# Performance work log

Hardware: AMD Instinct MI355X
Metric: run time of the kernel (lower is better)

## Reference

```python
import jax, jax.numpy as jnp
import numpy as np

N_FFT = 2048
HOP = 512
WIN_LENGTH = 2048
B, C, T, F = 8, 1, 2048, N_FFT // 2 + 1
LENGTH = HOP * (T - 1)  # 1048064


def _window():
    # scipy/librosa hann with fftbins=True (periodic); win_length == n_fft so pad_center is a no-op
    n = np.arange(WIN_LENGTH)
    return 0.5 - 0.5 * np.cos(2.0 * np.pi * n / WIN_LENGTH)


def _idft_mats():
    k = np.arange(N_FFT)
    ang = 2.0 * np.pi * np.outer(k, k) / N_FFT
    w = _window()
    Mr = np.cos(ang) / N_FFT * w[:, None]
    Mi = np.sin(ang) / N_FFT * w[:, None]
    return jnp.asarray(Mr, jnp.float32), jnp.asarray(Mi, jnp.float32)


_MR, _MI = _idft_mats()


def _window_sumsquare(n_frames):
    # librosa.filters.window_sumsquare with norm=None
    win_sq = _window() ** 2
    total = N_FFT + HOP * (n_frames - 1)
    ws = np.zeros(total)
    idx = (np.arange(n_frames)[:, None] * HOP + np.arange(N_FFT)).ravel()
    np.add.at(ws, idx, np.tile(win_sq, n_frames))
    return jnp.asarray(np.clip(ws, 1e-8, np.inf), jnp.float32)


def setup_inputs() -> dict:
    key = jax.random.key(0)
    k1, k2 = jax.random.split(key)
    real_stft = jax.random.normal(k1, (B, C, T, F), dtype=jnp.float32)
    imag_stft = jax.random.normal(k2, (B, C, T, F), dtype=jnp.float32)
    return {"real_stft": real_stft, "imag_stft": imag_stft, "length": LENGTH}


def reference(real_stft, imag_stft, length):
    b, c, t, f = real_stft.shape
    r = jnp.swapaxes(real_stft, 2, 3)   # (B, C, F, T)
    im = jnp.swapaxes(imag_stft, 2, 3)
    # 'reverse' conv: pick bins n_fft//2-1 .. 1 (conjugate-symmetric half)
    rev = slice(N_FFT // 2 - 1, 0, -1)
    full_r = jnp.concatenate([r, r[:, :, rev, :]], axis=2)        # (B, C, n_fft, T)
    full_i = jnp.concatenate([im, -im[:, :, rev, :]], axis=2)
    # windowed IDFT (real part of inverse transform), as the 1x1-conv matmuls do
    s = (jnp.einsum('ab,xcbt->xcta', _MR, full_r)
         - jnp.einsum('ab,xcbt->xcta', _MI, full_i))              # (B, C, T, n_fft)
    total = N_FFT + HOP * (t - 1)
    idx = jnp.arange(t)[:, None] * HOP + jnp.arange(N_FFT)        # (T, n_fft)
    # overlap-add (replaces the identity-kernel ConvTranspose2d)
    y = jnp.zeros((b, c, total), dtype=s.dtype).at[:, :, idx].add(s)
    y = y / _window_sumsquare(t)                                   # window-sum normalization
    start = N_FFT // 2                                             # center=True
    avail = total - start
    y = jax.lax.dynamic_slice_in_dim(y, start, min(length, avail), axis=2)
    if y.shape[-1] < length:
        y = jnp.pad(y, ((0, 0), (0, 0), (0, length - y.shape[-1])))
    return y  # (B, C, length)
```

## Files before the change

### kernel.cpp

```cpp
#include <hip/hip_runtime.h>

#define NFFT    2048
#define HOPSZ   512
#define BATCH   8
#define TFRAMES 2048
#define FBINS   1025
#define OUTLEN  1048064
#define TOTALP  1050112
#define MROWS   16384

__device__ __forceinline__ float bf2f(unsigned short h) {
    return __uint_as_float(((unsigned)h) << 16);
}

__device__ __forceinline__ float2 cmul(float2 a, float2 b) {
    return float2{a.x * b.x - a.y * b.y, a.x * b.y + a.y * b.x};
}
__device__ __forceinline__ float2 cadd(float2 a, float2 b) { return float2{a.x + b.x, a.y + b.y}; }
__device__ __forceinline__ float2 csub(float2 a, float2 b) { return float2{a.x - b.x, a.y - b.y}; }
__device__ __forceinline__ float2 cjmul(float2 a) { return float2{-a.y, a.x}; }

#define IDFT4(y0, y1, y2, y3, x0, x1, x2, x3) do {                         \
    float2 t0 = cadd(x0, x2), t1 = csub(x0, x2);                           \
    float2 t2 = cadd(x1, x3), t3 = cjmul(csub(x1, x3));                    \
    y0 = cadd(t0, t2); y2 = csub(t0, t2);                                  \
    y1 = cadd(t1, t3); y3 = csub(t1, t3); } while (0)

__device__ __forceinline__ void idft16(float2* y, const float2* x) {
    const float c1 = 0.92387953251128674f, s1 = 0.38268343236508977f;
    const float r2 = 0.70710678118654752f;
    float2 A[16];
    #pragma unroll
    for (int jb = 0; jb < 4; ++jb)
        IDFT4(A[jb * 4 + 0], A[jb * 4 + 1], A[jb * 4 + 2], A[jb * 4 + 3],
              x[jb], x[4 + jb], x[8 + jb], x[12 + jb]);
    A[4 + 1]  = cmul(A[4 + 1],  float2{c1, s1});
    A[4 + 2]  = cmul(A[4 + 2],  float2{r2, r2});
    A[4 + 3]  = cmul(A[4 + 3],  float2{s1, c1});
    A[8 + 1]  = cmul(A[8 + 1],  float2{r2, r2});
    A[8 + 2]  = cjmul(A[8 + 2]);
    A[8 + 3]  = cmul(A[8 + 3],  float2{-r2, r2});
    A[12 + 1] = cmul(A[12 + 1], float2{s1, c1});
    A[12 + 2] = cmul(A[12 + 2], float2{-r2, r2});
    A[12 + 3] = cmul(A[12 + 3], float2{-c1, -s1});
    #pragma unroll
    for (int ra = 0; ra < 4; ++ra)
        IDFT4(y[ra], y[ra + 4], y[ra + 8], y[ra + 12],
              A[ra], A[4 + ra], A[8 + ra], A[12 + ra]);
}

__global__ void build_tabs(float2* __restrict__ wt) {
    int n = blockIdx.x * 256 + threadIdx.x;
    const float s = 1.0f / 2048.0f;
    if (n < 1024)
        wt[n] = float2{(0.5f - 0.5f * cospif((float)(2 * n)     * (1.0f / 1024.0f))) * s,
                       (0.5f - 0.5f * cospif((float)(2 * n + 1) * (1.0f / 1024.0f))) * s};
}

__global__ __launch_bounds__(128) void fft_frames(
    const float* __restrict__ re, const float* __restrict__ im,
    const float2* __restrict__ wt,
    unsigned short* __restrict__ Y)
{
    __shared__ float2 tb[2][1024];

    const int tid   = threadIdx.x;
    const int lane  = tid & 63;
    const int wv    = tid >> 6;
    const int frame = blockIdx.x * 2 + wv;
    const int b     = frame >> 11;
    const int t     = frame & (TFRAMES - 1);
    const float* rr = re + (size_t)frame * FBINS;
    const float* ii = im + (size_t)frame * FBINS;

    const float2 packb = float2{cospif((float)lane * (1.0f / 1024.0f)),
                                sinpif((float)lane * (1.0f / 1024.0f))};
    const float2 base2 = cmul(packb, packb);

    const float wkc[16] = { 1.0f, 0.98078528040323044f, 0.92387953251128674f, 0.83146961230254524f,
                            0.70710678118654752f, 0.55557023301960222f, 0.38268343236508977f, 0.19509032201612827f,
                            0.0f, -0.19509032201612827f, -0.38268343236508977f, -0.55557023301960222f,
                            -0.70710678118654752f, -0.83146961230254524f, -0.92387953251128674f, -0.98078528040323044f };
    const float wks[16] = { 0.0f, 0.19509032201612827f, 0.38268343236508977f, 0.55557023301960222f,
                            0.70710678118654752f, 0.83146961230254524f, 0.92387953251128674f, 0.98078528040323044f,
                            1.0f, 0.98078528040323044f, 0.92387953251128674f, 0.83146961230254524f,
                            0.70710678118654752f, 0.55557023301960222f, 0.38268343236508977f, 0.19509032201612827f };

    float2 zz[16];
    #pragma unroll
    for (int k1 = 0; k1 < 16; ++k1) {
        const int m = 64 * k1 + lane;
        float Xr = rr[m],        Xi = ii[m];
        float Cr = rr[1024 - m], Ni = ii[1024 - m];
        float2 W = cmul(packb, float2{wkc[k1], wks[k1]});
        float Er = Xr + Cr, Ei = Xi - Ni;
        float Or = Xr - Cr, Oi = Xi + Ni;
        float2 z = float2{Er - (W.x * Oi + W.y * Or), Ei + (W.x * Or - W.y * Oi)};
        if (k1 == 0 && lane == 0)
            z = float2{Xr + Cr, Xr - Cr};
        zz[k1] = z;
    }

    float2 A[16];
    idft16(A, zz);

    {
        float2 w = base2;
        A[1] = cmul(A[1], w);
        #pragma unroll
        for (int n1 = 2; n1 < 16; ++n1) { w = cmul(w, base2); A[n1] = cmul(A[n1], w); }
    }

    {
        float4* rowp = (float4*)&tb[wv][lane * 16];
        #pragma unroll
        for (int j = 0; j < 8; ++j) {
            float2 e = A[2 * j], o = A[2 * j + 1];
            rowp[(j + lane) & 7] = float4{e.x, e.y, o.x, o.y};
        }
    }
    asm volatile("s_waitcnt lgkmcnt(0)" ::: "memory");
    __builtin_amdgcn_sched_barrier(0);

    const int q   = lane >> 4;
    const int n1r = lane & 15;
    float2 D[16];
    #pragma unroll
    for (int c1 = 0; c1 < 16; ++c1) {
        const int row = 4 * c1 + q;
        D[c1] = tb[wv][row * 16 + (((n1r >> 1) + row) & 7) * 2 + (n1r & 1)];
    }

    float2 E[16];
    idft16(E, D);

    {
        float2 bq = (q == 0) ? float2{1.0f, 0.0f}
                  : (q == 1) ? float2{0.99518472667219693f, 0.09801714032956060f}
                  : (q == 2) ? float2{0.98078528040323044f, 0.19509032201612827f}
                             : float2{0.95694033573220886f, 0.29028467725446237f};
        float2 w = bq;
        E[1] = cmul(E[1], w);
        #pragma unroll
        for (int v1 = 2; v1 < 16; ++v1) { w = cmul(w, bq); E[v1] = cmul(E[v1], w); }
    }

    unsigned short* Yb = Y + ((size_t)(b * 4 + (t & 3))) * TOTALP + t * HOPSZ;
    const int v2 = ((q & 1) << 1) | (q >> 1);
    const int nbase = n1r + (v2 << 8);
    #pragma unroll
    for (int v1 = 0; v1 < 16; ++v1) {
        float2 mine = E[v1];
        float2 oth  = float2{__shfl_xor(mine.x, 32), __shfl_xor(mine.y, 32)};
        float2 G    = (lane < 32) ? cadd(mine, oth) : csub(oth, mine);
        float2 o2   = float2{__shfl_xor(G.x, 16), __shfl_xor(G.y, 16)};
        float2 res;
        if (q == 0)      res = cadd(G, o2);
        else if (q == 1) res = csub(o2, G);
        else if (q == 2) res = float2{G.x - o2.y, G.y + o2.x};
        else             res = float2{o2.x + G.y, o2.y - G.x};
        const int n = nbase + (v1 << 4);
        const float2 wp = wt[n];
        const float lo = res.x * wp.x, hi = res.y * wp.y;
        unsigned pack;
        asm("v_cvt_pk_bf16_f32 %0, %1, %2" : "=v"(pack) : "v"(lo), "v"(hi));
        *(unsigned*)(Yb + 2 * n) = pack;
    }
}

__global__ __launch_bounds__(256) void final_pass(
    const unsigned short* __restrict__ Y,
    const float2*         __restrict__ wt,
    float*                __restrict__ out)
{
    const int tx = blockIdx.x * 256 + threadIdx.x;
    if (tx >= OUTLEN / 8) return;
    const int b  = blockIdx.y;
    const int n0 = tx * 8;
    const int p0 = n0 + 1024;
    int tmin = (p0 - 1536) >> 9;  if (tmin < 0) tmin = 0;
    int tmax = p0 >> 9;           if (tmax > TFRAMES - 1) tmax = TFRAMES - 1;

    float acc[8], ws[8];
    #pragma unroll
    for (int j = 0; j < 8; ++j) { acc[j] = 0.0f; ws[j] = 0.0f; }

    for (int t = tmin; t <= tmax; ++t) {
        const int a0 = p0 - t * HOPSZ;
        const uint4 pv = *(const uint4*)(Y + ((size_t)(b * 4 + (t & 3))) * TOTALP + p0);
        const unsigned pw[4] = {pv.x, pv.y, pv.z, pv.w};
        #pragma unroll
        for (int j = 0; j < 4; ++j) {
            acc[2 * j]     += bf2f((unsigned short)(pw[j] & 0xffffu));
            acc[2 * j + 1] += bf2f((unsigned short)(pw[j] >> 16));
        }
        #pragma unroll
        for (int j = 0; j < 4; ++j) {
            float2 w = wt[(a0 >> 1) + j];
            ws[2 * j]     += w.x * w.x;
            ws[2 * j + 1] += w.y * w.y;
        }
    }
    const float S2 = (1.0f / 2048.0f) * (1.0f / 2048.0f);
    float r[8];
    #pragma unroll
    for (int j = 0; j < 8; ++j) r[j] = acc[j] * S2 / fmaxf(ws[j], 2.4e-15f);
    float4* o = (float4*)(out + (size_t)b * OUTLEN + n0);
    o[0] = float4{r[0], r[1], r[2], r[3]};
    o[1] = float4{r[4], r[5], r[6], r[7]};
}

extern "C" void kernel_launch(void* const* d_in, const int* in_sizes, int n_in,
                              void* d_out, int out_size, void* d_ws, size_t ws_size,
                              hipStream_t stream) {
    const float* re = (const float*)d_in[0];
    const float* im = (const float*)d_in[1];
    float* out = (float*)d_out;

    char* ws = (char*)d_ws;
    unsigned short* Y  = (unsigned short*)(ws);
    float2*         wt = (float2*)       (ws + 67207168);

    build_tabs<<<dim3(4),          256, 0, stream>>>(wt);
    fft_frames<<<dim3(MROWS / 2),  128, 0, stream>>>(re, im, wt, Y);
    final_pass<<<dim3(512, BATCH), 256, 0, stream>>>(Y, wt, out);
}
```

Measured before the change: 76.41 us.

## Process two frames per wavefront with interleaved FFT stages

Each wavefront now handles two STFT frames instead of one, and the grid is halved to match. The code is split into helper stages so the second frame's global loads and first-stage FFT run between the first frame's LDS transpose and its second stage, overlapping memory latency with compute. The explicit waitcnt/sched barrier is dropped and the twiddle constants move to __constant__ memory. In exchange, register pressure rises under the (128,4) launch bound, which risks spills and lower occupancy.

```diff
diff --git a/kernel.cpp b/kernel.cpp
--- a/kernel.cpp
+++ b/kernel.cpp
@@ -49,6 +49,15 @@
               A[ra], A[4 + ra], A[8 + ra], A[12 + ra]);
 }
 
+__constant__ float WKC[16] = { 1.0f, 0.98078528040323044f, 0.92387953251128674f, 0.83146961230254524f,
+                               0.70710678118654752f, 0.55557023301960222f, 0.38268343236508977f, 0.19509032201612827f,
+                               0.0f, -0.19509032201612827f, -0.38268343236508977f, -0.55557023301960222f,
+                               -0.70710678118654752f, -0.83146961230254524f, -0.92387953251128674f, -0.98078528040323044f };
+__constant__ float WKS[16] = { 0.0f, 0.19509032201612827f, 0.38268343236508977f, 0.55557023301960222f,
+                               0.70710678118654752f, 0.83146961230254524f, 0.92387953251128674f, 0.98078528040323044f,
+                               1.0f, 0.98078528040323044f, 0.92387953251128674f, 0.83146961230254524f,
+                               0.70710678118654752f, 0.55557023301960222f, 0.38268343236508977f, 0.19509032201612827f };
+
 __global__ void build_tabs(float2* __restrict__ wt) {
     int n = blockIdx.x * 256 + threadIdx.x;
     const float s = 1.0f / 2048.0f;
@@ -57,42 +66,18 @@
                        (0.5f - 0.5f * cospif((float)(2 * n + 1) * (1.0f / 1024.0f))) * s};
 }
 
-__global__ __launch_bounds__(128) void fft_frames(
-    const float* __restrict__ re, const float* __restrict__ im,
-    const float2* __restrict__ wt,
-    unsigned short* __restrict__ Y)
-{
-    __shared__ float2 tb[2][1024];
-
-    const int tid   = threadIdx.x;
-    const int lane  = tid & 63;
-    const int wv    = tid >> 6;
-    const int frame = blockIdx.x * 2 + wv;
-    const int b     = frame >> 11;
-    const int t     = frame & (TFRAMES - 1);
-    const float* rr = re + (size_t)frame * FBINS;
-    const float* ii = im + (size_t)frame * FBINS;
-
-    const float2 packb = float2{cospif((float)lane * (1.0f / 1024.0f)),
-                                sinpif((float)lane * (1.0f / 1024.0f))};
-    const float2 base2 = cmul(packb, packb);
-
-    const float wkc[16] = { 1.0f, 0.98078528040323044f, 0.92387953251128674f, 0.83146961230254524f,
-                            0.70710678118654752f, 0.55557023301960222f, 0.38268343236508977f, 0.19509032201612827f,
-                            0.0f, -0.19509032201612827f, -0.38268343236508977f, -0.55557023301960222f,
-                            -0.70710678118654752f, -0.83146961230254524f, -0.92387953251128674f, -0.98078528040323044f };
-    const float wks[16] = { 0.0f, 0.19509032201612827f, 0.38268343236508977f, 0.55557023301960222f,
-                            0.70710678118654752f, 0.83146961230254524f, 0.92387953251128674f, 0.98078528040323044f,
-                            1.0f, 0.98078528040323044f, 0.92387953251128674f, 0.83146961230254524f,
-                            0.70710678118654752f, 0.55557023301960222f, 0.38268343236508977f, 0.19509032201612827f };
-
+__device__ __forceinline__ void stage12(const float* __restrict__ rr,
+                                        const float* __restrict__ ii,
+                                        int lane, float2 packb, float2 base2,
+                                        float2* __restrict__ A)
+{
     float2 zz[16];
     #pragma unroll
     for (int k1 = 0; k1 < 16; ++k1) {
         const int m = 64 * k1 + lane;
         float Xr = rr[m],        Xi = ii[m];
         float Cr = rr[1024 - m], Ni = ii[1024 - m];
-        float2 W = cmul(packb, float2{wkc[k1], wks[k1]});
+        float2 W = cmul(packb, float2{WKC[k1], WKS[k1]});
         float Er = Xr + Cr, Ei = Xi - Ni;
         float Or = Xr - Cr, Oi = Xi + Ni;
         float2 z = float2{Er - (W.x * Oi + W.y * Or), Ei + (W.x * Or - W.y * Oi)};
@@ -100,52 +85,49 @@
             z = float2{Xr + Cr, Xr - Cr};
         zz[k1] = z;
     }
-
-    float2 A[16];
     idft16(A, zz);
-
-    {
-        float2 w = base2;
-        A[1] = cmul(A[1], w);
-        #pragma unroll
-        for (int n1 = 2; n1 < 16; ++n1) { w = cmul(w, base2); A[n1] = cmul(A[n1], w); }
-    }
-
-    {
-        float4* rowp = (float4*)&tb[wv][lane * 16];
-        #pragma unroll
-        for (int j = 0; j < 8; ++j) {
-            float2 e = A[2 * j], o = A[2 * j + 1];
-            rowp[(j + lane) & 7] = float4{e.x, e.y, o.x, o.y};
-        }
-    }
-    asm volatile("s_waitcnt lgkmcnt(0)" ::: "memory");
-    __builtin_amdgcn_sched_barrier(0);
-
-    const int q   = lane >> 4;
-    const int n1r = lane & 15;
+    float2 w = base2;
+    A[1] = cmul(A[1], w);
+    #pragma unroll
+    for (int n1 = 2; n1 < 16; ++n1) { w = cmul(w, base2); A[n1] = cmul(A[n1], w); }
+}
+
+__device__ __forceinline__ void stage3(const float2* __restrict__ tbw,
+                                       int q, int n1r, float2* __restrict__ E)
+{
     float2 D[16];
     #pragma unroll
     for (int c1 = 0; c1 < 16; ++c1) {
         const int row = 4 * c1 + q;
-        D[c1] = tb[wv][row * 16 + (((n1r >> 1) + row) & 7) * 2 + (n1r & 1)];
-    }
-
-    float2 E[16];
+        D[c1] = tbw[row * 16 + (((n1r >> 1) + row) & 7) * 2 + (n1r & 1)];
+    }
     idft16(E, D);
-
-    {
-        float2 bq = (q == 0) ? float2{1.0f, 0.0f}
-                  : (q == 1) ? float2{0.99518472667219693f, 0.09801714032956060f}
-                  : (q == 2) ? float2{0.98078528040323044f, 0.19509032201612827f}
-                             : float2{0.95694033573220886f, 0.29028467725446237f};
-        float2 w = bq;
-        E[1] = cmul(E[1], w);
-        #pragma unroll
-        for (int v1 = 2; v1 < 16; ++v1) { w = cmul(w, bq); E[v1] = cmul(E[v1], w); }
-    }
-
-    unsigned short* Yb = Y + ((size_t)(b * 4 + (t & 3))) * TOTALP + t * HOPSZ;
+    float2 bq = (q == 0) ? float2{1.0f, 0.0f}
+              : (q == 1) ? float2{0.99518472667219693f, 0.09801714032956060f}
+              : (q == 2) ? float2{0.98078528040323044f, 0.19509032201612827f}
+                         : float2{0.95694033573220886f, 0.29028467725446237f};
+    float2 w = bq;
+    E[1] = cmul(E[1], w);
+    #pragma unroll
+    for (int v1 = 2; v1 < 16; ++v1) { w = cmul(w, bq); E[v1] = cmul(E[v1], w); }
+}
+
+__device__ __forceinline__ void twrite(float2* __restrict__ tbw, int lane,
+                                       const float2* __restrict__ A)
+{
+    float4* rowp = (float4*)&tbw[lane * 16];
+    #pragma unroll
+    for (int j = 0; j < 8; ++j) {
+        float2 e = A[2 * j], o = A[2 * j + 1];
+        rowp[(j + lane) & 7] = float4{e.x, e.y, o.x, o.y};
+    }
+}
+
+__device__ __forceinline__ void tailstore(const float2* __restrict__ E,
+                                          int lane, int q, int n1r,
+                                          const float2* __restrict__ wt,
+                                          unsigned short* __restrict__ Yb)
+{
     const int v2 = ((q & 1) << 1) | (q >> 1);
     const int nbase = n1r + (v2 << 8);
     #pragma unroll
@@ -168,6 +150,59 @@
     }
 }
 
+__global__ __launch_bounds__(128, 4) void fft_frames(
+    const float* __restrict__ re, const float* __restrict__ im,
+    const float2* __restrict__ wt,
+    unsigned short* __restrict__ Y)
+{
+    __shared__ float2 tb[2][1024];
+
+    const int tid   = threadIdx.x;
+    const int lane  = tid & 63;
+    const int wv    = tid >> 6;
+    const int fA    = blockIdx.x * 4 + wv * 2;
+    const int fB    = fA + 1;
+    float2* tbw     = tb[wv];
+
+    const float2 packb = float2{cospif((float)lane * (1.0f / 1024.0f)),
+                                sinpif((float)lane * (1.0f / 1024.0f))};
+    const float2 base2 = cmul(packb, packb);
+
+    const int q   = lane >> 4;
+    const int n1r = lane & 15;
+
+    const float* rrA = re + (size_t)fA * FBINS;
+    const float* iiA = im + (size_t)fA * FBINS;
+    const float* rrB = re + (size_t)fB * FBINS;
+    const float* iiB = im + (size_t)fB * FBINS;
+
+    float2 AA[16];
+    stage12(rrA, iiA, lane, packb, base2, AA);
+    twrite(tbw, lane, AA);
+
+    float2 AB[16];
+    stage12(rrB, iiB, lane, packb, base2, AB);
+
+    float2 EA[16];
+    stage3(tbw, q, n1r, EA);
+
+    twrite(tbw, lane, AB);
+
+    {
+        const int b = fA >> 11, t = fA & (TFRAMES - 1);
+        unsigned short* Yb = Y + ((size_t)(b * 4 + (t & 3))) * TOTALP + t * HOPSZ;
+        tailstore(EA, lane, q, n1r, wt, Yb);
+    }
+
+    float2 EB[16];
+    stage3(tbw, q, n1r, EB);
+    {
+        const int b = fB >> 11, t = fB & (TFRAMES - 1);
+        unsigned short* Yb = Y + ((size_t)(b * 4 + (t & 3))) * TOTALP + t * HOPSZ;
+        tailstore(EB, lane, q, n1r, wt, Yb);
+    }
+}
+
 __global__ __launch_bounds__(256) void final_pass(
     const unsigned short* __restrict__ Y,
     const float2*         __restrict__ wt,
@@ -222,6 +257,6 @@
     float2*         wt = (float2*)       (ws + 67207168);
 
     build_tabs<<<dim3(4),          256, 0, stream>>>(wt);
-    fft_frames<<<dim3(MROWS / 2),  128, 0, stream>>>(re, im, wt, Y);
+    fft_frames<<<dim3(MROWS / 4),  128, 0, stream>>>(re, im, wt, Y);
     final_pass<<<dim3(512, BATCH), 256, 0, stream>>>(Y, wt, out);
 }
```

Result: slower. 294.3 us (+285.1%).

## Precompute twiddle tables, use packed float2 math, and fast-path interior overlap-add normalization

Applied to the files above, without the earlier changes.

Switches complex arithmetic to ext_vector float2 so the compiler can emit packed FP32 instructions. Replaces the per-thread twiddle recurrences and cospif/sinpif calls with lookups into precomputed twiddle tables built once per call. In the final pass, interior samples take an unrolled four-frame path with the constant Hann window-sum (1.5, folded into a 2/3 factor) instead of accumulating window squares. This trades ALU work for extra global table loads, and the constant normalization assumes exactly four overlapping frames per interior sample.

```diff
diff --git a/kernel.cpp b/kernel.cpp
--- a/kernel.cpp
+++ b/kernel.cpp
@@ -9,60 +9,77 @@
 #define TOTALP  1050112
 #define MROWS   16384
 
+
+typedef float f2 __attribute__((ext_vector_type(2)));
+
 __device__ __forceinline__ float bf2f(unsigned short h) {
     return __uint_as_float(((unsigned)h) << 16);
 }
 
-__device__ __forceinline__ float2 cmul(float2 a, float2 b) {
-    return float2{a.x * b.x - a.y * b.y, a.x * b.y + a.y * b.x};
-}
-__device__ __forceinline__ float2 cadd(float2 a, float2 b) { return float2{a.x + b.x, a.y + b.y}; }
-__device__ __forceinline__ float2 csub(float2 a, float2 b) { return float2{a.x - b.x, a.y - b.y}; }
-__device__ __forceinline__ float2 cjmul(float2 a) { return float2{-a.y, a.x}; }
+__device__ __forceinline__ f2 cmul(f2 a, f2 b) {
+    f2 r = a * f2{b.x, b.x};
+    return __builtin_shufflevector(a, a, 1, 0) * f2{-b.y, b.y} + r;
+}
+__device__ __forceinline__ f2 cjmul(f2 a) {
+    return __builtin_shufflevector(a, a, 1, 0) * f2{-1.0f, 1.0f};
+}
 
 #define IDFT4(y0, y1, y2, y3, x0, x1, x2, x3) do {                         \
-    float2 t0 = cadd(x0, x2), t1 = csub(x0, x2);                           \
-    float2 t2 = cadd(x1, x3), t3 = cjmul(csub(x1, x3));                    \
-    y0 = cadd(t0, t2); y2 = csub(t0, t2);                                  \
-    y1 = cadd(t1, t3); y3 = csub(t1, t3); } while (0)
-
-__device__ __forceinline__ void idft16(float2* y, const float2* x) {
+    f2 t0 = x0 + x2, t1 = x0 - x2;                                         \
+    f2 t2 = x1 + x3, jd = cjmul(x1 - x3);                                  \
+    y0 = t0 + t2; y2 = t0 - t2;                                            \
+    y1 = t1 + jd; y3 = t1 - jd; } while (0)
+
+__device__ __forceinline__ void idft16(f2* y, const f2* x) {
     const float c1 = 0.92387953251128674f, s1 = 0.38268343236508977f;
     const float r2 = 0.70710678118654752f;
-    float2 A[16];
+    f2 A[16];
     #pragma unroll
     for (int jb = 0; jb < 4; ++jb)
         IDFT4(A[jb * 4 + 0], A[jb * 4 + 1], A[jb * 4 + 2], A[jb * 4 + 3],
               x[jb], x[4 + jb], x[8 + jb], x[12 + jb]);
-    A[4 + 1]  = cmul(A[4 + 1],  float2{c1, s1});
-    A[4 + 2]  = cmul(A[4 + 2],  float2{r2, r2});
-    A[4 + 3]  = cmul(A[4 + 3],  float2{s1, c1});
-    A[8 + 1]  = cmul(A[8 + 1],  float2{r2, r2});
+    A[4 + 1]  = cmul(A[4 + 1],  f2{c1, s1});
+    A[4 + 2]  = cmul(A[4 + 2],  f2{r2, r2});
+    A[4 + 3]  = cmul(A[4 + 3],  f2{s1, c1});
+    A[8 + 1]  = cmul(A[8 + 1],  f2{r2, r2});
     A[8 + 2]  = cjmul(A[8 + 2]);
-    A[8 + 3]  = cmul(A[8 + 3],  float2{-r2, r2});
-    A[12 + 1] = cmul(A[12 + 1], float2{s1, c1});
-    A[12 + 2] = cmul(A[12 + 2], float2{-r2, r2});
-    A[12 + 3] = cmul(A[12 + 3], float2{-c1, -s1});
+    A[8 + 3]  = cmul(A[8 + 3],  f2{-r2, r2});
+    A[12 + 1] = cmul(A[12 + 1], f2{s1, c1});
+    A[12 + 2] = cmul(A[12 + 2], f2{-r2, r2});
+    A[12 + 3] = cmul(A[12 + 3], f2{-c1, -s1});
     #pragma unroll
     for (int ra = 0; ra < 4; ++ra)
         IDFT4(y[ra], y[ra + 4], y[ra + 8], y[ra + 12],
               A[ra], A[4 + ra], A[8 + ra], A[12 + ra]);
 }
 
-__global__ void build_tabs(float2* __restrict__ wt) {
-    int n = blockIdx.x * 256 + threadIdx.x;
+__global__ void build_tabs(f2* __restrict__ tabs) {
+    int i = blockIdx.x * 256 + threadIdx.x;
     const float s = 1.0f / 2048.0f;
-    if (n < 1024)
-        wt[n] = float2{(0.5f - 0.5f * cospif((float)(2 * n)     * (1.0f / 1024.0f))) * s,
-                       (0.5f - 0.5f * cospif((float)(2 * n + 1) * (1.0f / 1024.0f))) * s};
+    if (i < 1024) {
+        tabs[i] = f2{(0.5f - 0.5f * cospif((float)(2 * i)     * (1.0f / 1024.0f))) * s,
+                     (0.5f - 0.5f * cospif((float)(2 * i + 1) * (1.0f / 1024.0f))) * s};
+    } else if (i < 2048) {
+        int j = i - 1024, n1 = j >> 6, l = j & 63;
+        float ang = (float)(n1 * l) * (1.0f / 512.0f);
+        tabs[i] = f2{cospif(ang), sinpif(ang)};
+    } else if (i < 2112) {
+        int j = i - 2048, qq = j >> 4, v1 = j & 15;
+        float ang = (float)(qq * v1) * (1.0f / 32.0f);
+        tabs[i] = f2{cospif(ang), sinpif(ang)};
+    } else if (i < 3136) {
+        int m = i - 2112;
+        tabs[i] = f2{cospif((float)m * (1.0f / 1024.0f)),
+                     sinpif((float)m * (1.0f / 1024.0f))};
+    }
 }
 
 __global__ __launch_bounds__(128) void fft_frames(
     const float* __restrict__ re, const float* __restrict__ im,
-    const float2* __restrict__ wt,
+    const f2* __restrict__ tabs,
     unsigned short* __restrict__ Y)
 {
-    __shared__ float2 tb[2][1024];
+    __shared__ f2 tb[2][1024];
 
     const int tid   = threadIdx.x;
     const int lane  = tid & 63;
@@ -72,50 +89,40 @@
     const int t     = frame & (TFRAMES - 1);
     const float* rr = re + (size_t)frame * FBINS;
     const float* ii = im + (size_t)frame * FBINS;
-
-    const float2 packb = float2{cospif((float)lane * (1.0f / 1024.0f)),
-                                sinpif((float)lane * (1.0f / 1024.0f))};
-    const float2 base2 = cmul(packb, packb);
-
-    const float wkc[16] = { 1.0f, 0.98078528040323044f, 0.92387953251128674f, 0.83146961230254524f,
-                            0.70710678118654752f, 0.55557023301960222f, 0.38268343236508977f, 0.19509032201612827f,
-                            0.0f, -0.19509032201612827f, -0.38268343236508977f, -0.55557023301960222f,
-                            -0.70710678118654752f, -0.83146961230254524f, -0.92387953251128674f, -0.98078528040323044f };
-    const float wks[16] = { 0.0f, 0.19509032201612827f, 0.38268343236508977f, 0.55557023301960222f,
-                            0.70710678118654752f, 0.83146961230254524f, 0.92387953251128674f, 0.98078528040323044f,
-                            1.0f, 0.98078528040323044f, 0.92387953251128674f, 0.83146961230254524f,
-                            0.70710678118654752f, 0.55557023301960222f, 0.38268343236508977f, 0.19509032201612827f };
-
-    float2 zz[16];
+    f2* tbw         = tb[wv];
+
+    const f2* WT  = tabs;
+    const f2* T2  = tabs + 1024;
+    const f2* T64 = tabs + 2048;
+    const f2* TP  = tabs + 2112;
+
+    f2 zz[16];
     #pragma unroll
     for (int k1 = 0; k1 < 16; ++k1) {
         const int m = 64 * k1 + lane;
-        float Xr = rr[m],        Xi = ii[m];
-        float Cr = rr[1024 - m], Ni = ii[1024 - m];
-        float2 W = cmul(packb, float2{wkc[k1], wks[k1]});
-        float Er = Xr + Cr, Ei = Xi - Ni;
-        float Or = Xr - Cr, Oi = Xi + Ni;
-        float2 z = float2{Er - (W.x * Oi + W.y * Or), Ei + (W.x * Or - W.y * Oi)};
+        f2 X  = f2{rr[m],        ii[m]};
+        f2 M  = f2{rr[1024 - m], ii[1024 - m]};
+        f2 Cc = M * f2{1.0f, -1.0f};
+        f2 E  = X + Cc;
+        f2 O  = X - Cc;
+        f2 z  = E + cjmul(cmul(TP[m], O));
         if (k1 == 0 && lane == 0)
-            z = float2{Xr + Cr, Xr - Cr};
+            z = f2{X.x + M.x, X.x - M.x};
         zz[k1] = z;
     }
 
-    float2 A[16];
+    f2 A[16];
     idft16(A, zz);
 
+    #pragma unroll
+    for (int n1 = 1; n1 < 16; ++n1)
+        A[n1] = cmul(A[n1], T2[n1 * 64 + lane]);
+
     {
-        float2 w = base2;
-        A[1] = cmul(A[1], w);
-        #pragma unroll
-        for (int n1 = 2; n1 < 16; ++n1) { w = cmul(w, base2); A[n1] = cmul(A[n1], w); }
-    }
-
-    {
-        float4* rowp = (float4*)&tb[wv][lane * 16];
+        float4* rowp = (float4*)&tbw[lane * 16];
         #pragma unroll
         for (int j = 0; j < 8; ++j) {
-            float2 e = A[2 * j], o = A[2 * j + 1];
+            f2 e = A[2 * j], o = A[2 * j + 1];
             rowp[(j + lane) & 7] = float4{e.x, e.y, o.x, o.y};
         }
     }
@@ -124,53 +131,45 @@
 
     const int q   = lane >> 4;
     const int n1r = lane & 15;
-    float2 D[16];
+    f2 D[16];
     #pragma unroll
     for (int c1 = 0; c1 < 16; ++c1) {
         const int row = 4 * c1 + q;
-        D[c1] = tb[wv][row * 16 + (((n1r >> 1) + row) & 7) * 2 + (n1r & 1)];
-    }
-
-    float2 E[16];
+        D[c1] = tbw[row * 16 + (((n1r >> 1) + row) & 7) * 2 + (n1r & 1)];
+    }
+
+    f2 E[16];
     idft16(E, D);
 
-    {
-        float2 bq = (q == 0) ? float2{1.0f, 0.0f}
-                  : (q == 1) ? float2{0.99518472667219693f, 0.09801714032956060f}
-                  : (q == 2) ? float2{0.98078528040323044f, 0.19509032201612827f}
-                             : float2{0.95694033573220886f, 0.29028467725446237f};
-        float2 w = bq;
-        E[1] = cmul(E[1], w);
-        #pragma unroll
-        for (int v1 = 2; v1 < 16; ++v1) { w = cmul(w, bq); E[v1] = cmul(E[v1], w); }
-    }
+    #pragma unroll
+    for (int v1 = 1; v1 < 16; ++v1)
+        E[v1] = cmul(E[v1], T64[q * 16 + v1]);
 
     unsigned short* Yb = Y + ((size_t)(b * 4 + (t & 3))) * TOTALP + t * HOPSZ;
     const int v2 = ((q & 1) << 1) | (q >> 1);
     const int nbase = n1r + (v2 << 8);
     #pragma unroll
     for (int v1 = 0; v1 < 16; ++v1) {
-        float2 mine = E[v1];
-        float2 oth  = float2{__shfl_xor(mine.x, 32), __shfl_xor(mine.y, 32)};
-        float2 G    = (lane < 32) ? cadd(mine, oth) : csub(oth, mine);
-        float2 o2   = float2{__shfl_xor(G.x, 16), __shfl_xor(G.y, 16)};
-        float2 res;
-        if (q == 0)      res = cadd(G, o2);
-        else if (q == 1) res = csub(o2, G);
-        else if (q == 2) res = float2{G.x - o2.y, G.y + o2.x};
-        else             res = float2{o2.x + G.y, o2.y - G.x};
+        f2 mine = E[v1];
+        f2 oth  = f2{__shfl_xor(mine.x, 32), __shfl_xor(mine.y, 32)};
+        f2 G    = (lane < 32) ? (mine + oth) : (oth - mine);
+        f2 o2   = f2{__shfl_xor(G.x, 16), __shfl_xor(G.y, 16)};
+        f2 res;
+        if (q == 0)      res = G + o2;
+        else if (q == 1) res = o2 - G;
+        else if (q == 2) res = G + cjmul(o2);
+        else             res = o2 - cjmul(G);
         const int n = nbase + (v1 << 4);
-        const float2 wp = wt[n];
-        const float lo = res.x * wp.x, hi = res.y * wp.y;
+        f2 rw = res * WT[n];
         unsigned pack;
-        asm("v_cvt_pk_bf16_f32 %0, %1, %2" : "=v"(pack) : "v"(lo), "v"(hi));
+        asm("v_cvt_pk_bf16_f32 %0, %1, %2" : "=v"(pack) : "v"(rw.x), "v"(rw.y));
         *(unsigned*)(Yb + 2 * n) = pack;
     }
 }
 
 __global__ __launch_bounds__(256) void final_pass(
     const unsigned short* __restrict__ Y,
-    const float2*         __restrict__ wt,
+    const f2*             __restrict__ tabs,
     float*                __restrict__ out)
 {
     const int tx = blockIdx.x * 256 + threadIdx.x;
@@ -178,13 +177,39 @@
     const int b  = blockIdx.y;
     const int n0 = tx * 8;
     const int p0 = n0 + 1024;
+
+    float acc[8];
+    #pragma unroll
+    for (int j = 0; j < 8; ++j) acc[j] = 0.0f;
+
+    if (p0 >= 1536 && p0 < 1048576) {
+        const int tmin = (p0 - 1536) >> 9;
+        #pragma unroll
+        for (int k = 0; k < 4; ++k) {
+            const int t = tmin + k;
+            const uint4 pv = *(const uint4*)(Y + ((size_t)(b * 4 + (t & 3))) * TOTALP + p0);
+            const unsigned pw[4] = {pv.x, pv.y, pv.z, pv.w};
+            #pragma unroll
+            for (int j = 0; j < 4; ++j) {
+                acc[2 * j]     += bf2f((unsigned short)(pw[j] & 0xffffu));
+                acc[2 * j + 1] += bf2f((unsigned short)(pw[j] >> 16));
+            }
+        }
+        const float inv = 2.0f / 3.0f;
+        float r[8];
+        #pragma unroll
+        for (int j = 0; j < 8; ++j) r[j] = acc[j] * inv;
+        float4* o = (float4*)(out + (size_t)b * OUTLEN + n0);
+        o[0] = float4{r[0], r[1], r[2], r[3]};
+        o[1] = float4{r[4], r[5], r[6], r[7]};
+        return;
+    }
+
     int tmin = (p0 - 1536) >> 9;  if (tmin < 0) tmin = 0;
     int tmax = p0 >> 9;           if (tmax > TFRAMES - 1) tmax = TFRAMES - 1;
-
-    float acc[8], ws[8];
-    #pragma unroll
-    for (int j = 0; j < 8; ++j) { acc[j] = 0.0f; ws[j] = 0.0f; }
-
+    float ws[8];
+    #pragma unroll
+    for (int j = 0; j < 8; ++j) ws[j] = 0.0f;
     for (int t = tmin; t <= tmax; ++t) {
         const int a0 = p0 - t * HOPSZ;
         const uint4 pv = *(const uint4*)(Y + ((size_t)(b * 4 + (t & 3))) * TOTALP + p0);
@@ -196,7 +221,7 @@
         }
         #pragma unroll
         for (int j = 0; j < 4; ++j) {
-            float2 w = wt[(a0 >> 1) + j];
+            f2 w = tabs[(a0 >> 1) + j];
             ws[2 * j]     += w.x * w.x;
             ws[2 * j + 1] += w.y * w.y;
         }
@@ -218,10 +243,10 @@
     float* out = (float*)d_out;
 
     char* ws = (char*)d_ws;
-    unsigned short* Y  = (unsigned short*)(ws);
-    float2*         wt = (float2*)       (ws + 67207168);
-
-    build_tabs<<<dim3(4),          256, 0, stream>>>(wt);
-    fft_frames<<<dim3(MROWS / 2),  128, 0, stream>>>(re, im, wt, Y);
-    final_pass<<<dim3(512, BATCH), 256, 0, stream>>>(Y, wt, out);
-}
+    unsigned short* Y    = (unsigned short*)(ws);
+    f2*             tabs = (f2*)           (ws + 67207168);
+
+    build_tabs<<<dim3(13),         256, 0, stream>>>(tabs);
+    fft_frames<<<dim3(MROWS / 2),  128, 0, stream>>>(re, im, tabs, Y);
+    final_pass<<<dim3(512, BATCH), 256, 0, stream>>>(Y, tabs, out);
+}
```

Result: slower. 82.37 us (+7.8%).
